# Performance work log

Hardware: AMD Instinct MI355X
Metric: run time of the kernel (lower is better)

The kernel has to match this reference:

```python
import jax, jax.numpy as jnp
import numpy as np

D_MODEL = 1024
N_HEADS = 16
D_K = D_MODEL // N_HEADS
D_FF = 4096
B, S = 2, 2048
EPS = 1e-5


def setup_inputs() -> dict:
    key = jax.random.key(0)
    ks = jax.random.split(key, 16)
    sc = 0.02
    inp = {
        'x': jax.random.normal(ks[0], (B, S, D_MODEL), dtype=jnp.float32),
        'mask': jnp.ones((B, 1, 1, S), dtype=jnp.int32),
        'Wq': jax.random.normal(ks[1], (D_MODEL, D_MODEL), dtype=jnp.float32) * sc,
        'bq': jnp.zeros((D_MODEL,), dtype=jnp.float32),
        'Wk': jax.random.normal(ks[2], (D_MODEL, D_MODEL), dtype=jnp.float32) * sc,
        'bk': jnp.zeros((D_MODEL,), dtype=jnp.float32),
        'Wv': jax.random.normal(ks[3], (D_MODEL, D_MODEL), dtype=jnp.float32) * sc,
        'bv': jnp.zeros((D_MODEL,), dtype=jnp.float32),
        'Wo': jax.random.normal(ks[4], (D_MODEL, D_MODEL), dtype=jnp.float32) * sc,
        'bo': jnp.zeros((D_MODEL,), dtype=jnp.float32),
        'W1': jax.random.normal(ks[5], (D_MODEL, D_FF), dtype=jnp.float32) * sc,
        'b1': jnp.zeros((D_FF,), dtype=jnp.float32),
        'W2': jax.random.normal(ks[6], (D_FF, D_MODEL), dtype=jnp.float32) * sc,
        'b2': jnp.zeros((D_MODEL,), dtype=jnp.float32),
        'g1': jnp.ones((D_MODEL,), dtype=jnp.float32),
        'be1': jnp.zeros((D_MODEL,), dtype=jnp.float32),
        'g2': jnp.ones((D_MODEL,), dtype=jnp.float32),
        'be2': jnp.zeros((D_MODEL,), dtype=jnp.float32),
    }
    return inp


def _layernorm(x, g, b):
    mu = jnp.mean(x, axis=-1, keepdims=True)
    var = jnp.mean(jnp.square(x - mu), axis=-1, keepdims=True)
    return (x - mu) * jax.lax.rsqrt(var + EPS) * g + b


def _split_heads(x):
    b, s, _ = x.shape
    return x.reshape(b, s, N_HEADS, D_K).transpose(0, 2, 1, 3)  # [B,H,S,Dk]


def reference(x, mask, Wq, bq, Wk, bk, Wv, bv, Wo, bo, W1, b1, W2, b2, g1, be1, g2, be2):
    Q = _split_heads(x @ Wq + bq)
    K = _split_heads(x @ Wk + bk)
    V = _split_heads(x @ Wv + bv)
    scores = jnp.einsum('bhqd,bhkd->bhqk', Q, K) / jnp.sqrt(jnp.float32(D_K))
    scores = jnp.where(mask == 0, -jnp.inf, scores)
    attn = jax.nn.softmax(scores, axis=-1)
    ctx = jnp.einsum('bhqk,bhkd->bhqd', attn, V)
    ctx = ctx.transpose(0, 2, 1, 3).reshape(x.shape[0], x.shape[1], D_MODEL)
    attn_out = ctx @ Wo + bo
    h = _layernorm(x + attn_out, g1, be1)
    ff = jax.nn.relu(h @ W1 + b1) @ W2 + b2
    return _layernorm(h + ff, g2, be2)
```

## Files before the change

### kernel.cpp

```cpp
#include <hip/hip_runtime.h>
#include <hip/hip_bf16.h>

#define D_MODELC 1024
#define D_FFC    4096
#define N_HEADSC 16
#define BATCHC   2
#define SEQC     2048
#define M_TOK    (BATCHC*SEQC)

typedef __attribute__((ext_vector_type(4)))  float f32x4;
typedef __attribute__((ext_vector_type(16))) float f32x16;
typedef __attribute__((ext_vector_type(8)))  short s16x8;
using bf16_t = __hip_bfloat16;

static __device__ __forceinline__ unsigned short f2bf_u16(float f) {
  bf16_t h = __float2bfloat16(f);
  return __builtin_bit_cast(unsigned short, h);
}

static __device__ __forceinline__ unsigned int cvt_pk_bf16(float lo, float hi2) {
  unsigned int r;
  asm("v_cvt_pk_bf16_f32 %0, %1, %2" : "=v"(r) : "v"(lo), "v"(hi2));
  return r;
}

#define PSWAP(a, b) asm volatile("v_permlane32_swap_b32 %0, %1" : "+v"(a), "+v"(b))

#define ASYNC_COPY16(dst_lds, src_g) \
  __builtin_amdgcn_global_load_lds((const __attribute__((address_space(1))) void*)(src_g), \
                                   (__attribute__((address_space(3))) void*)(dst_lds), 16, 0, 0)

__global__ __launch_bounds__(256) void k_transpose_f32_bf16(
    const float* __restrict__ in, bf16_t* __restrict__ out, int R, int C) {
  __shared__ float tile[32][33];
  int tx = threadIdx.x & 31, ty = threadIdx.x >> 5;
  int c0 = blockIdx.x * 32, r0 = blockIdx.y * 32;
#pragma unroll
  for (int i = 0; i < 4; ++i)
    tile[ty + i * 8][tx] = in[(size_t)(r0 + ty + i * 8) * C + c0 + tx];
  __syncthreads();
#pragma unroll
  for (int i = 0; i < 4; ++i)
    out[(size_t)(c0 + ty + i * 8) * R + r0 + tx] = __float2bfloat16(tile[tx][ty + i * 8]);
}

__global__ __launch_bounds__(256) void k_f32_to_bf16(
    const float* __restrict__ in, bf16_t* __restrict__ out, int n4) {
  int i = blockIdx.x * 256 + threadIdx.x;
  if (i < n4) {
    float4 v = ((const float4*)in)[i];
    short4 o;
    o.x = (short)f2bf_u16(v.x);
    o.y = (short)f2bf_u16(v.y);
    o.z = (short)f2bf_u16(v.z);
    o.w = (short)f2bf_u16(v.w);
    ((short4*)out)[i] = o;
  }
}

__global__ __launch_bounds__(256) void k_pack_bias(
    const float* __restrict__ bq, const float* __restrict__ bk,
    const float* __restrict__ bv, float* __restrict__ out) {
  int i = blockIdx.x * 256 + threadIdx.x;
  float v = (i < 1024) ? bq[i] : (i < 2048) ? bk[i - 1024] : bv[i - 2048];
  out[i] = v;
}

#define GBK 64

__global__ __launch_bounds__(256, 2) void k_gemm(
    const bf16_t* __restrict__ A, const bf16_t* __restrict__ BT,
    const float* __restrict__ bias,
    float* __restrict__ p0, float* __restrict__ p1,
    void* __restrict__ Cout, int M, int N, int K,
    int lda, int ldb, int ldc, int mode, int nsplit) {
  __shared__ __align__(16) bf16_t Asm[128 * GBK];
  __shared__ __align__(16) bf16_t Bsm[128 * GBK];

  const int nbn = N / 128;
  const int nwg = gridDim.x;
  const int cpx = nwg >> 3;
  int wg = (blockIdx.x & 7) * cpx + (blockIdx.x >> 3);
  int kslice = 0;
  if (nsplit == 2) { kslice = wg & 1; wg >>= 1; }
  const int mb = wg / nbn, nb = wg % nbn;
  const int row0 = mb * 128, col0 = nb * 128;
  A  += (size_t)kslice * K;
  BT += (size_t)kslice * K;

  const int tid = threadIdx.x;
  const int w = tid >> 6, lane = tid & 63;
  const int lr = lane & 15, lg = lane >> 4;
  const int wr = w >> 1, wc = w & 1;
  const int wbase = tid & 192;

  f32x4 acc[4][4];
#pragma unroll
  for (int m = 0; m < 4; ++m)
#pragma unroll
    for (int n = 0; n < 4; ++n) acc[m][n] = (f32x4){0.f, 0.f, 0.f, 0.f};

  for (int k0 = 0; k0 < K; k0 += GBK) {
    __syncthreads();
#pragma unroll
    for (int i = 0; i < 4; ++i) {
      int c = i * 256 + tid;
      int row = c >> 3;
      int sg = (c & 7) ^ (row & 7);
      ASYNC_COPY16(Asm + (size_t)(i * 256 + wbase) * 8,
                   A + (size_t)(row0 + row) * lda + k0 + sg * 8);
    }
#pragma unroll
    for (int i = 0; i < 4; ++i) {
      int c = i * 256 + tid;
      int row = c >> 3;
      int sg = (c & 7) ^ (row & 7);
      ASYNC_COPY16(Bsm + (size_t)(i * 256 + wbase) * 8,
                   BT + (size_t)(col0 + row) * ldb + k0 + sg * 8);
    }
    __syncthreads();
#pragma unroll
    for (int kst = 0; kst < 2; ++kst) {
      const int sl = ((kst * 4 + lg) ^ (lr & 7)) * 8;
      s16x8 af[4], bfr[4];
#pragma unroll
      for (int m = 0; m < 4; ++m)
        af[m] = *(const s16x8*)(Asm + (size_t)(wr * 64 + m * 16 + lr) * GBK + sl);
#pragma unroll
      for (int n = 0; n < 4; ++n)
        bfr[n] = *(const s16x8*)(Bsm + (size_t)(wc * 64 + n * 16 + lr) * GBK + sl);
#pragma unroll
      for (int m = 0; m < 4; ++m)
#pragma unroll
        for (int n = 0; n < 4; ++n)
          acc[m][n] = __builtin_amdgcn_mfma_f32_16x16x32_bf16(af[m], bfr[n], acc[m][n], 0, 0, 0);
    }
  }

  float* outf = (kslice == 0) ? p0 : p1;
  bf16_t* outh = (bf16_t*)Cout;
#pragma unroll
  for (int m = 0; m < 4; ++m) {
    int grow = row0 + wr * 64 + m * 16 + lg * 4;
#pragma unroll
    for (int n = 0; n < 4; ++n) {
      int gcol = col0 + wc * 64 + n * 16 + lr;
      float bv = (mode == 4) ? 0.f : bias[gcol];
      float cs = (mode == 3 && gcol < 1024) ? 0.18033688f : 1.f;
#pragma unroll
      for (int r = 0; r < 4; ++r) {
        float v = (acc[m][n][r] + bv) * cs;
        size_t idx = (size_t)(grow + r) * ldc + gcol;
        if (mode == 4) {
          outf[idx] = v;
        } else {
          if (mode == 1) v = fmaxf(v, 0.f);
          outh[idx] = __float2bfloat16(v);
        }
      }
    }
  }
}

__global__ __launch_bounds__(256, 2) void k_attn(
    const bf16_t* __restrict__ qkv, const int* __restrict__ mask,
    bf16_t* __restrict__ ctx) {
  const int bid = blockIdx.x;
  const int qt = bid & 15;
  const int h  = (bid >> 4) & 15;
  const int b  = bid >> 8;
  const int tid = threadIdx.x;
  const int w = tid >> 6, lane = tid & 63;
  const int l31 = lane & 31, hi = lane >> 5;
  const int wbase = tid & 192;

  __shared__ __align__(16) bf16_t Kl[2][64][64];
  __shared__ __align__(16) bf16_t Vl[2][4096];
  __shared__ __align__(16) float  mskf[2][68];

  const int tokb = b * SEQC;
  const int q0 = qt * 128 + w * 32;

  s16x8 qfrag[4];
  {
    const bf16_t* qp = qkv + (size_t)(tokb + q0 + l31) * 3072 + h * 64 + hi * 8;
#pragma unroll
    for (int s = 0; s < 4; ++s) qfrag[s] = *(const s16x8*)(qp + s * 16);
  }

  char* klc = (char*)&Kl[0][0][0];
  bf16_t* Vl0 = &Vl[0][0];
  const unsigned vbase =
      (unsigned)(size_t)(__attribute__((address_space(3))) bf16_t*)Vl0 + lane * 8;

  float mreg = 1.f;

#define STAGE_K(buf, kb)                                                              \
  {                                                                                   \
    _Pragma("unroll")                                                                 \
    for (int ii = 0; ii < 2; ++ii) {                                                  \
      int chunk = w * 2 + ii;                                                         \
      int row = chunk * 8 + (lane >> 3);                                              \
      int seg = (lane & 7) ^ (row & 7);                                               \
      const bf16_t* src = qkv + (size_t)(tokb + (kb) + row) * 3072 + 1024 + h * 64 + seg * 8; \
      ASYNC_COPY16(&Kl[buf][chunk * 8][0], src);                                      \
    }                                                                                 \
  }

#define STAGE_V(buf, kb)                                                              \
  {                                                                                   \
    _Pragma("unroll")                                                                 \
    for (int ii = 0; ii < 2; ++ii) {                                                  \
      const int c = tid + ii * 256;                                                   \
      const int L = c >> 3;                                                           \
      const int vf_ = L >> 4, vt_ = (L >> 3) & 1, vdb_ = (L >> 2) & 1;                \
      const int vh_ = (L >> 1) & 1, vdo_ = L & 1;                                     \
      const int vkey = 16 * vf_ + 8 * vh_ + 4 * vt_ + ((c & 7) >> 1);                 \
      const int vd = ((vdb_ * 2 + vdo_) << 4) + (c & 1) * 8;                          \
      const bf16_t* vsrc = qkv + (size_t)(tokb + (kb) + vkey) * 3072 + 2048 + h * 64 + vd; \
      ASYNC_COPY16(Vl0 + (size_t)(buf) * 4096 + (size_t)(ii * 256 + wbase) * 8, vsrc); \
    }                                                                                 \
  }

#define STAGE_M(buf, kb)                                                              \
  {                                                                                   \
    if (w == 0) {                                                                     \
      mreg = mask[tokb + (kb) + lane] ? 1.f : 0.f;                                    \
      mskf[buf][lane] = mreg;                                                         \
      unsigned long long z = __ballot(mreg == 0.f);                                   \
      if (lane == 0) mskf[buf][64] = (z == 0ull) ? 1.f : 0.f;                         \
    }                                                                                 \
  }

  STAGE_K(0, 0)
  STAGE_V(0, 0)
  STAGE_M(0, 0)

  f32x16 o[2];
#pragma unroll
  for (int d = 0; d < 2; ++d)
#pragma unroll
    for (int i = 0; i < 16; ++i) o[d][i] = 0.f;
  float psum = 0.f;

  __syncthreads();

  for (int kt = 0; kt < SEQC / 64; ++kt) {
    const int kb = kt * 64;
    const int cur = kt & 1, nxt = cur ^ 1;
    const bool more = (kt < SEQC / 64 - 1);

    if (more) {
      STAGE_K(nxt, kb + 64)
      STAGE_V(nxt, kb + 64)
      STAGE_M(nxt, kb + 64)
    }

    f32x16 st[2];
#pragma unroll
    for (int kk = 0; kk < 2; ++kk)
#pragma unroll
      for (int i = 0; i < 16; ++i) st[kk][i] = 0.f;
#pragma unroll
    for (int step = 0; step < 4; ++step) {
#pragma unroll
      for (int kb2 = 0; kb2 < 2; ++kb2) {
        int key = kb2 * 32 + l31;
        int seg = (2 * step + hi) ^ (lane & 7);
        s16x8 kf = *(const s16x8*)(klc + cur * 8192 + key * 128 + seg * 16);
        st[kb2] = __builtin_amdgcn_mfma_f32_32x32x16_bf16(kf, qfrag[step], st[kb2], 0, 0, 0);
      }
    }

    const unsigned va = vbase + cur * 8192;
    ulong tr[4][2][2];
#pragma unroll
    for (int f = 0; f < 4; ++f)
#pragma unroll
      for (int db = 0; db < 2; ++db)
        asm volatile("ds_read_b64_tr_b16 %0, %2 offset:%c3\n\t"
                     "ds_read_b64_tr_b16 %1, %2 offset:%c4"
                     : "=v"(tr[f][db][0]), "=v"(tr[f][db][1])
                     : "v"(va), "i"((f * 16 + db * 4) * 128), "i"((f * 16 + 8 + db * 4) * 128));

    const bool allv = (mskf[cur][64] != 0.f);
    s16x8 pf[4];
#pragma unroll
    for (int kb2 = 0; kb2 < 2; ++kb2) {
      float pa[16];
      if (allv) {
#pragma unroll
        for (int i = 0; i < 16; ++i) {
          float e = __builtin_exp2f(st[kb2][i]);
          pa[i] = e;
          psum += e;
        }
      } else {
#pragma unroll
        for (int g = 0; g < 4; ++g) {
          f32x4 mm = *(const f32x4*)((char*)&mskf[cur][0] + (kb2 * 128 + g * 32 + hi * 16));
#pragma unroll
          for (int rr = 0; rr < 4; ++rr) {
            float e = __builtin_exp2f(st[kb2][g * 4 + rr]) * mm[rr];
            pa[g * 4 + rr] = e;
            psum += e;
          }
        }
      }
      unsigned int wv[8];
#pragma unroll
      for (int u = 0; u < 8; ++u) wv[u] = cvt_pk_bf16(pa[2 * u], pa[2 * u + 1]);
      unsigned int a0 = wv[0], b0 = wv[2]; PSWAP(a0, b0);
      unsigned int a1 = wv[1], b1 = wv[3]; PSWAP(a1, b1);
      unsigned int a2 = wv[4], b2 = wv[6]; PSWAP(a2, b2);
      unsigned int a3 = wv[5], b3 = wv[7]; PSWAP(a3, b3);
      uint4 u0 = {a0, a1, b0, b1};
      uint4 u1 = {a2, a3, b2, b3};
      pf[kb2 * 2 + 0] = __builtin_bit_cast(s16x8, u0);
      pf[kb2 * 2 + 1] = __builtin_bit_cast(s16x8, u1);
    }

    asm volatile("s_waitcnt lgkmcnt(0)" ::: "memory");
    __builtin_amdgcn_sched_barrier(0);
#pragma unroll
    for (int f = 0; f < 4; ++f)
#pragma unroll
      for (int db = 0; db < 2; ++db) {
        ulong2 uv = {tr[f][db][0], tr[f][db][1]};
        s16x8 vfr = __builtin_bit_cast(s16x8, uv);
        o[db] = __builtin_amdgcn_mfma_f32_32x32x16_bf16(pf[f], vfr, o[db], 0, 0, 0);
      }

    __syncthreads();
  }

  psum += __shfl_xor(psum, 32);
  float rs[16];
#pragma unroll
  for (int r = 0; r < 16; ++r) {
    int qq = (r & 3) + 8 * (r >> 2) + 4 * hi;
    rs[r] = __shfl(psum, qq);
  }
#pragma unroll
  for (int dblk = 0; dblk < 2; ++dblk)
#pragma unroll
    for (int r = 0; r < 16; ++r) {
      int qq = (r & 3) + 8 * (r >> 2) + 4 * hi;
      int tok = tokb + q0 + qq;
      ctx[(size_t)tok * 1024 + h * 64 + dblk * 32 + l31] = __float2bfloat16(o[dblk][r] / rs[r]);
    }
#undef STAGE_K
#undef STAGE_V
#undef STAGE_M
}

__global__ __launch_bounds__(256) void k_ln_res2(
    const float* __restrict__ p0, const float* __restrict__ p1,
    const float* __restrict__ res, const float* __restrict__ bias,
    const float* __restrict__ g, const float* __restrict__ be,
    float* __restrict__ outf, bf16_t* __restrict__ outh) {
  const int row = blockIdx.x, tid = threadIdx.x;
  const size_t base = (size_t)row * D_MODELC;
  const float4 a  = ((const float4*)(p0 + base))[tid];
  const float4 bq = ((const float4*)(p1 + base))[tid];
  const float4 c  = ((const float4*)(res + base))[tid];
  const float4 bi = ((const float4*)bias)[tid];
  float4 v;
  v.x = a.x + bq.x + c.x + bi.x;
  v.y = a.y + bq.y + c.y + bi.y;
  v.z = a.z + bq.z + c.z + bi.z;
  v.w = a.w + bq.w + c.w + bi.w;
  float s1 = v.x + v.y + v.z + v.w;
  float s2 = v.x * v.x + v.y * v.y + v.z * v.z + v.w * v.w;
#pragma unroll
  for (int mm = 1; mm < 64; mm <<= 1) {
    s1 += __shfl_xor(s1, mm);
    s2 += __shfl_xor(s2, mm);
  }
  __shared__ float sa[4], sb[4];
  const int wv = tid >> 6;
  if ((tid & 63) == 0) { sa[wv] = s1; sb[wv] = s2; }
  __syncthreads();
  s1 = sa[0] + sa[1] + sa[2] + sa[3];
  s2 = sb[0] + sb[1] + sb[2] + sb[3];
  const float mu = s1 * (1.f / D_MODELC);
  const float var = s2 * (1.f / D_MODELC) - mu * mu;
  const float rsq = rsqrtf(var + 1e-5f);
  const float4 gg = ((const float4*)g)[tid];
  const float4 bb = ((const float4*)be)[tid];
  float4 oo;
  oo.x = (v.x - mu) * rsq * gg.x + bb.x;
  oo.y = (v.y - mu) * rsq * gg.y + bb.y;
  oo.z = (v.z - mu) * rsq * gg.z + bb.z;
  oo.w = (v.w - mu) * rsq * gg.w + bb.w;
  ((float4*)(outf + base))[tid] = oo;
  if (outh) {
    short4 ob;
    ob.x = (short)f2bf_u16(oo.x);
    ob.y = (short)f2bf_u16(oo.y);
    ob.z = (short)f2bf_u16(oo.z);
    ob.w = (short)f2bf_u16(oo.w);
    ((short4*)(outh + base))[tid] = ob;
  }
}

extern "C" void kernel_launch(void* const* d_in, const int* in_sizes, int n_in,
                              void* d_out, int out_size, void* d_ws, size_t ws_size,
                              hipStream_t stream) {
  (void)in_sizes; (void)n_in; (void)out_size; (void)ws_size;
  const float* x   = (const float*)d_in[0];
  const int* mask  = (const int*)d_in[1];
  const float* Wq  = (const float*)d_in[2];
  const float* bq  = (const float*)d_in[3];
  const float* Wk  = (const float*)d_in[4];
  const float* bk  = (const float*)d_in[5];
  const float* Wv  = (const float*)d_in[6];
  const float* bv  = (const float*)d_in[7];
  const float* Wo  = (const float*)d_in[8];
  const float* bo  = (const float*)d_in[9];
  const float* W1  = (const float*)d_in[10];
  const float* b1  = (const float*)d_in[11];
  const float* W2  = (const float*)d_in[12];
  const float* b2  = (const float*)d_in[13];
  const float* g1  = (const float*)d_in[14];
  const float* be1 = (const float*)d_in[15];
  const float* g2  = (const float*)d_in[16];
  const float* be2 = (const float*)d_in[17];

  char* ws = (char*)d_ws;
  const size_t D = D_MODELC, F = D_FFC, M = M_TOK;
  const size_t SZ_X16  = M * D * 2;
  const size_t SZ_QKV  = M * 3 * D * 2;
  bf16_t* x16   = (bf16_t*)ws;
  bf16_t* ff1   = (bf16_t*)ws;
  bf16_t* qkvb  = (bf16_t*)(ws + SZ_X16);
  size_t off = SZ_X16 + SZ_QKV;
  bf16_t* ctx   = (bf16_t*)(ws + off); off += M * D * 2;
  bf16_t* wqkvT = (bf16_t*)(ws + off); off += 3 * D * D * 2;
  bf16_t* woT   = (bf16_t*)(ws + off); off += D * D * 2;
  bf16_t* w1T   = (bf16_t*)(ws + off); off += D * F * 2;
  bf16_t* w2T   = (bf16_t*)(ws + off); off += D * F * 2;
  float*  partA = (float*)(ws + off);  off += M * D * 4;
  float*  hbuf  = (float*)(ws + off);  off += M * D * 4;
  bf16_t* h16   = (bf16_t*)(ws + off); off += M * D * 2;
  float*  partB = (float*)(ws + off);  off += M * D * 4;
  float*  bqkv  = (float*)(ws + off);  off += 3 * D * 4;

  k_transpose_f32_bf16<<<dim3(32, 32), 256, 0, stream>>>(Wq, wqkvT, 1024, 1024);
  k_transpose_f32_bf16<<<dim3(32, 32), 256, 0, stream>>>(Wk, wqkvT + 1024 * 1024, 1024, 1024);
  k_transpose_f32_bf16<<<dim3(32, 32), 256, 0, stream>>>(Wv, wqkvT + 2 * 1024 * 1024, 1024, 1024);
  k_transpose_f32_bf16<<<dim3(32, 32), 256, 0, stream>>>(Wo, woT, 1024, 1024);
  k_transpose_f32_bf16<<<dim3(128, 32), 256, 0, stream>>>(W1, w1T, 1024, 4096);
  k_transpose_f32_bf16<<<dim3(32, 128), 256, 0, stream>>>(W2, w2T, 4096, 1024);
  k_f32_to_bf16<<<4096, 256, 0, stream>>>(x, x16, (int)(M * D / 4));
  k_pack_bias<<<12, 256, 0, stream>>>(bq, bk, bv, bqkv);

  k_gemm<<<768, 256, 0, stream>>>(x16, wqkvT, bqkv, nullptr, nullptr, qkvb,
                                  4096, 3072, 1024, 1024, 1024, 3072, 3, 1);

  k_attn<<<BATCHC * N_HEADSC * (SEQC / 128), 256, 0, stream>>>(qkvb, mask, ctx);

  k_gemm<<<512, 256, 0, stream>>>(ctx, woT, nullptr, partA, partB, nullptr,
                                  4096, 1024, 512, 1024, 1024, 1024, 4, 2);
  k_ln_res2<<<4096, 256, 0, stream>>>(partA, partB, x, bo, g1, be1, hbuf, h16);

  k_gemm<<<1024, 256, 0, stream>>>(h16, w1T, b1, nullptr, nullptr, ff1,
                                   4096, 4096, 1024, 1024, 1024, 4096, 1, 1);
  k_gemm<<<512, 256, 0, stream>>>(ff1, w2T, nullptr, partA, partB, nullptr,
                                  4096, 1024, 2048, 4096, 4096, 1024, 4, 2);
  k_ln_res2<<<4096, 256, 0, stream>>>(partA, partB, hbuf, b2, g2, be2, (float*)d_out, nullptr);
}
```

Baseline: 268.9 us.

## Split attention over key halves with merge kernel, batch small weight transposes

Attention now splits the key sequence into two halves, launching twice as many blocks (1024) and raising the occupancy hint to 4 blocks per SM. Each half writes unnormalized fp32 partial outputs and row sums, and a new merge kernel adds them and normalizes into bf16 ctx. This is valid without max subtraction because the kernel already uses a fixed scale with no running max. V transpose reads are also split per d-block to cut register pressure, and the four 1024x1024 weight transposes are fused into one launch. The cost is extra fp32 partial traffic plus one more kernel launch.

Measured after the change: 260.0 us. 3.3% less time.

```diff
diff --git a/kernel.cpp b/kernel.cpp
--- a/kernel.cpp
+++ b/kernel.cpp
@@ -29,6 +29,26 @@
 #define ASYNC_COPY16(dst_lds, src_g) \
   __builtin_amdgcn_global_load_lds((const __attribute__((address_space(1))) void*)(src_g), \
                                    (__attribute__((address_space(3))) void*)(dst_lds), 16, 0, 0)
+
+__global__ __launch_bounds__(256) void k_transpose4(
+    const float* __restrict__ s0, const float* __restrict__ s1,
+    const float* __restrict__ s2, const float* __restrict__ s3,
+    bf16_t* __restrict__ d0, bf16_t* __restrict__ d1,
+    bf16_t* __restrict__ d2, bf16_t* __restrict__ d3) {
+  const int z = blockIdx.z;
+  const float* in = (z == 0) ? s0 : (z == 1) ? s1 : (z == 2) ? s2 : s3;
+  bf16_t* out = (z == 0) ? d0 : (z == 1) ? d1 : (z == 2) ? d2 : d3;
+  __shared__ float tile[32][33];
+  int tx = threadIdx.x & 31, ty = threadIdx.x >> 5;
+  int c0 = blockIdx.x * 32, r0 = blockIdx.y * 32;
+#pragma unroll
+  for (int i = 0; i < 4; ++i)
+    tile[ty + i * 8][tx] = in[(size_t)(r0 + ty + i * 8) * 1024 + c0 + tx];
+  __syncthreads();
+#pragma unroll
+  for (int i = 0; i < 4; ++i)
+    out[(size_t)(c0 + ty + i * 8) * 1024 + r0 + tx] = __float2bfloat16(tile[tx][ty + i * 8]);
+}
 
 __global__ __launch_bounds__(256) void k_transpose_f32_bf16(
     const float* __restrict__ in, bf16_t* __restrict__ out, int R, int C) {
@@ -162,13 +182,16 @@
   }
 }
 
-__global__ __launch_bounds__(256, 2) void k_attn(
+__global__ __launch_bounds__(256, 4) void k_attn(
     const bf16_t* __restrict__ qkv, const int* __restrict__ mask,
-    bf16_t* __restrict__ ctx) {
+    float* __restrict__ pA, float* __restrict__ pB,
+    float* __restrict__ psA, float* __restrict__ psB) {
   const int bid = blockIdx.x;
-  const int qt = bid & 15;
-  const int h  = (bid >> 4) & 15;
-  const int b  = bid >> 8;
+  const int half = bid >> 9;
+  const int inner = bid & 511;
+  const int qt = inner & 15;
+  const int h  = (inner >> 4) & 15;
+  const int b  = inner >> 8;
   const int tid = threadIdx.x;
   const int w = tid >> 6, lane = tid & 63;
   const int l31 = lane & 31, hi = lane >> 5;
@@ -180,6 +203,7 @@
 
   const int tokb = b * SEQC;
   const int q0 = qt * 128 + w * 32;
+  const int kb0 = half * (SEQC / 2);
 
   s16x8 qfrag[4];
   {
@@ -232,9 +256,9 @@
     }                                                                                 \
   }
 
-  STAGE_K(0, 0)
-  STAGE_V(0, 0)
-  STAGE_M(0, 0)
+  STAGE_K(0, kb0)
+  STAGE_V(0, kb0)
+  STAGE_M(0, kb0)
 
   f32x16 o[2];
 #pragma unroll
@@ -245,10 +269,10 @@
 
   __syncthreads();
 
-  for (int kt = 0; kt < SEQC / 64; ++kt) {
-    const int kb = kt * 64;
+  for (int kt = 0; kt < SEQC / 128; ++kt) {
+    const int kb = kb0 + kt * 64;
     const int cur = kt & 1, nxt = cur ^ 1;
-    const bool more = (kt < SEQC / 64 - 1);
+    const bool more = (kt < SEQC / 128 - 1);
 
     if (more) {
       STAGE_K(nxt, kb + 64)
@@ -271,17 +295,6 @@
         st[kb2] = __builtin_amdgcn_mfma_f32_32x32x16_bf16(kf, qfrag[step], st[kb2], 0, 0, 0);
       }
     }
-
-    const unsigned va = vbase + cur * 8192;
-    ulong tr[4][2][2];
-#pragma unroll
-    for (int f = 0; f < 4; ++f)
-#pragma unroll
-      for (int db = 0; db < 2; ++db)
-        asm volatile("ds_read_b64_tr_b16 %0, %2 offset:%c3\n\t"
-                     "ds_read_b64_tr_b16 %1, %2 offset:%c4"
-                     : "=v"(tr[f][db][0]), "=v"(tr[f][db][1])
-                     : "v"(va), "i"((f * 16 + db * 4) * 128), "i"((f * 16 + 8 + db * 4) * 128));
 
     const bool allv = (mskf[cur][64] != 0.f);
     s16x8 pf[4];
@@ -320,38 +333,64 @@
       pf[kb2 * 2 + 1] = __builtin_bit_cast(s16x8, u1);
     }
 
-    asm volatile("s_waitcnt lgkmcnt(0)" ::: "memory");
-    __builtin_amdgcn_sched_barrier(0);
-#pragma unroll
-    for (int f = 0; f < 4; ++f)
-#pragma unroll
-      for (int db = 0; db < 2; ++db) {
-        ulong2 uv = {tr[f][db][0], tr[f][db][1]};
+    const unsigned va = vbase + cur * 8192;
+#pragma unroll
+    for (int db = 0; db < 2; ++db) {
+      ulong tr[4][2];
+#pragma unroll
+      for (int f = 0; f < 4; ++f)
+        asm volatile("ds_read_b64_tr_b16 %0, %2 offset:%c3\n\t"
+                     "ds_read_b64_tr_b16 %1, %2 offset:%c4"
+                     : "=v"(tr[f][0]), "=v"(tr[f][1])
+                     : "v"(va), "i"((f * 16 + db * 4) * 128), "i"((f * 16 + 8 + db * 4) * 128));
+      asm volatile("s_waitcnt lgkmcnt(0)" ::: "memory");
+      __builtin_amdgcn_sched_barrier(0);
+#pragma unroll
+      for (int f = 0; f < 4; ++f) {
+        ulong2 uv = {tr[f][0], tr[f][1]};
         s16x8 vfr = __builtin_bit_cast(s16x8, uv);
         o[db] = __builtin_amdgcn_mfma_f32_32x32x16_bf16(pf[f], vfr, o[db], 0, 0, 0);
       }
+    }
 
     __syncthreads();
   }
 
   psum += __shfl_xor(psum, 32);
-  float rs[16];
-#pragma unroll
-  for (int r = 0; r < 16; ++r) {
-    int qq = (r & 3) + 8 * (r >> 2) + 4 * hi;
-    rs[r] = __shfl(psum, qq);
-  }
+  float* po = half ? pB : pA;
+  float* ps = half ? psB : psA;
 #pragma unroll
   for (int dblk = 0; dblk < 2; ++dblk)
 #pragma unroll
     for (int r = 0; r < 16; ++r) {
       int qq = (r & 3) + 8 * (r >> 2) + 4 * hi;
       int tok = tokb + q0 + qq;
-      ctx[(size_t)tok * 1024 + h * 64 + dblk * 32 + l31] = __float2bfloat16(o[dblk][r] / rs[r]);
-    }
+      po[(size_t)tok * 1024 + h * 64 + dblk * 32 + l31] = o[dblk][r];
+    }
+  if (hi == 0)
+    ps[(size_t)(tokb + q0 + l31) * 16 + h] = psum;
 #undef STAGE_K
 #undef STAGE_V
 #undef STAGE_M
+}
+
+__global__ __launch_bounds__(256) void k_attn_merge(
+    const float* __restrict__ pA, const float* __restrict__ pB,
+    const float* __restrict__ psA, const float* __restrict__ psB,
+    bf16_t* __restrict__ ctx) {
+  const int row = blockIdx.x, tid = threadIdx.x;
+  const size_t base = (size_t)row * 1024;
+  const float4 a = ((const float4*)(pA + base))[tid];
+  const float4 b = ((const float4*)(pB + base))[tid];
+  const int hh = tid >> 4;
+  const float rs = psA[row * 16 + hh] + psB[row * 16 + hh];
+  const float inv = 1.f / rs;
+  short4 ob;
+  ob.x = (short)f2bf_u16((a.x + b.x) * inv);
+  ob.y = (short)f2bf_u16((a.y + b.y) * inv);
+  ob.z = (short)f2bf_u16((a.z + b.z) * inv);
+  ob.w = (short)f2bf_u16((a.w + b.w) * inv);
+  ((short4*)(ctx + base))[tid] = ob;
 }
 
 __global__ __launch_bounds__(256) void k_ln_res2(
@@ -445,11 +484,11 @@
   bf16_t* h16   = (bf16_t*)(ws + off); off += M * D * 2;
   float*  partB = (float*)(ws + off);  off += M * D * 4;
   float*  bqkv  = (float*)(ws + off);  off += 3 * D * 4;
-
-  k_transpose_f32_bf16<<<dim3(32, 32), 256, 0, stream>>>(Wq, wqkvT, 1024, 1024);
-  k_transpose_f32_bf16<<<dim3(32, 32), 256, 0, stream>>>(Wk, wqkvT + 1024 * 1024, 1024, 1024);
-  k_transpose_f32_bf16<<<dim3(32, 32), 256, 0, stream>>>(Wv, wqkvT + 2 * 1024 * 1024, 1024, 1024);
-  k_transpose_f32_bf16<<<dim3(32, 32), 256, 0, stream>>>(Wo, woT, 1024, 1024);
+  float*  psA   = (float*)(ws + off);  off += M * 16 * 4;
+  float*  psB   = (float*)(ws + off);  off += M * 16 * 4;
+
+  k_transpose4<<<dim3(32, 32, 4), 256, 0, stream>>>(
+      Wq, Wk, Wv, Wo, wqkvT, wqkvT + 1024 * 1024, wqkvT + 2 * 1024 * 1024, woT);
   k_transpose_f32_bf16<<<dim3(128, 32), 256, 0, stream>>>(W1, w1T, 1024, 4096);
   k_transpose_f32_bf16<<<dim3(32, 128), 256, 0, stream>>>(W2, w2T, 4096, 1024);
   k_f32_to_bf16<<<4096, 256, 0, stream>>>(x, x16, (int)(M * D / 4));
@@ -458,7 +497,8 @@
   k_gemm<<<768, 256, 0, stream>>>(x16, wqkvT, bqkv, nullptr, nullptr, qkvb,
                                   4096, 3072, 1024, 1024, 1024, 3072, 3, 1);
 
-  k_attn<<<BATCHC * N_HEADSC * (SEQC / 128), 256, 0, stream>>>(qkvb, mask, ctx);
+  k_attn<<<1024, 256, 0, stream>>>(qkvb, mask, partA, partB, psA, psB);
+  k_attn_merge<<<4096, 256, 0, stream>>>(partA, partB, psA, psB, ctx);
 
   k_gemm<<<512, 256, 0, stream>>>(ctx, woT, nullptr, partA, partB, nullptr,
                                   4096, 1024, 512, 1024, 1024, 1024, 4, 2);
```
